# Optimization experiments

Measured on AMD Instinct MI355X. Metric: run time of the kernel, lower is better.

Reference implementation:

```python
import jax, jax.numpy as jnp
import numpy as np

D = 512; H = 8; DFF = 2048; S1 = 1024; S2 = 512; B = 8; EPS = 1e-5


def setup_inputs() -> dict:
    key = jax.random.key(0)
    ks = jax.random.split(key, 10)
    def w(k, shape):
        return jax.random.normal(k, shape, dtype=jnp.float32) * 0.02
    return {
        "rna_embed": jax.random.normal(ks[0], (S1, B, D), dtype=jnp.float32),
        "protein_embed": jax.random.normal(ks[1], (S2, B, D), dtype=jnp.float32),
        # self-attention params (torch MHA packed in_proj)
        "Wqkv_s": w(ks[2], (3 * D, D)), "bqkv_s": jnp.zeros((3 * D,), jnp.float32),
        "Wo_s": w(ks[3], (D, D)), "bo_s": jnp.zeros((D,), jnp.float32),
        # cross-attention params
        "Wqkv_c": w(ks[4], (3 * D, D)), "bqkv_c": jnp.zeros((3 * D,), jnp.float32),
        "Wo_c": w(ks[5], (D, D)), "bo_c": jnp.zeros((D,), jnp.float32),
        # FFN params
        "W1": w(ks[6], (DFF, D)), "b1": jnp.zeros((DFF,), jnp.float32),
        "W2": w(ks[7], (D, DFF)), "b2": jnp.zeros((D,), jnp.float32),
        # LayerNorm params: norm0_1, norm1_1, norm1_2, norm2
        "g0": jnp.ones((D,), jnp.float32), "be0": jnp.zeros((D,), jnp.float32),
        "g11": jnp.ones((D,), jnp.float32), "be11": jnp.zeros((D,), jnp.float32),
        "g12": jnp.ones((D,), jnp.float32), "be12": jnp.zeros((D,), jnp.float32),
        "g2": jnp.ones((D,), jnp.float32), "be2": jnp.zeros((D,), jnp.float32),
    }


def _layernorm(x, g, b):
    m = jnp.mean(x, axis=-1, keepdims=True)
    v = jnp.mean(jnp.square(x - m), axis=-1, keepdims=True)
    return (x - m) * jax.lax.rsqrt(v + EPS) * g + b


def _mha(xq, xkv, Wqkv, bqkv, Wo, bo):
    # xq: (Sq, B, D), xkv: (Sk, B, D)
    Wq, Wk, Wv = jnp.split(Wqkv, 3, axis=0)
    bq, bk, bv = jnp.split(bqkv, 3)
    hd = D // H
    scale = 1.0 / np.sqrt(hd).astype(np.float32)
    q = (xq @ Wq.T + bq).reshape(xq.shape[0], -1, H, hd)   # (Sq,B,H,hd)
    k = (xkv @ Wk.T + bk).reshape(xkv.shape[0], -1, H, hd)  # (Sk,B,H,hd)
    v = (xkv @ Wv.T + bv).reshape(xkv.shape[0], -1, H, hd)
    scores = jnp.einsum('qbhd,kbhd->bhqk', q, k) * scale    # (B,H,Sq,Sk)
    attn = jax.nn.softmax(scores, axis=-1)
    o = jnp.einsum('bhqk,kbhd->qbhd', attn, v).reshape(xq.shape[0], -1, D)
    return o @ Wo.T + bo


def reference(rna_embed, protein_embed, Wqkv_s, bqkv_s, Wo_s, bo_s,
              Wqkv_c, bqkv_c, Wo_c, bo_c, W1, b1, W2, b2,
              g0, be0, g11, be11, g12, be12, g2, be2):
    x1 = rna_embed
    # pre-norm self-attention
    h = _layernorm(x1, g0, be0)
    x1 = x1 + _mha(h, h, Wqkv_s, bqkv_s, Wo_s, bo_s)
    # pre-norm cross-attention (queries from x1, keys/values from protein)
    x1 = x1 + _mha(_layernorm(x1, g11, be11), _layernorm(protein_embed, g12, be12),
                   Wqkv_c, bqkv_c, Wo_c, bo_c)
    # pre-norm FFN
    h = _layernorm(x1, g2, be2)
    x1 = x1 + (jax.nn.relu(h @ W1.T + b1) @ W2.T + b2)
    return x1
```

## Files before the change

kernel.cpp:

```cpp
#include <hip/hip_runtime.h>

typedef unsigned short u16;
typedef unsigned int u32;
typedef u16 u16x8 __attribute__((ext_vector_type(8)));
typedef u16 u16x4 __attribute__((ext_vector_type(4)));
typedef short bfx8 __attribute__((ext_vector_type(8)));
typedef float f32x4 __attribute__((ext_vector_type(4)));

#define AS1 __attribute__((address_space(1)))
#define AS3 __attribute__((address_space(3)))

__device__ __forceinline__ u16 f2bf(float f) {
  union { float f; u32 u; } c; c.f = f;
  u32 u = c.u;
  u += 0x7fffu + ((u >> 16) & 1u);
  return (u16)(u >> 16);
}

__device__ __forceinline__ u32 cvt_pk_bf16(float lo, float hi) {
  u32 r;
  asm("v_cvt_pk_bf16_f32 %0, %1, %2" : "=v"(r) : "v"(lo), "v"(hi));
  return r;
}

__device__ __forceinline__ float fexp2(float x) {
  float r;
  asm("v_exp_f32 %0, %1" : "=v"(r) : "v"(x));
  return r;
}

__device__ __forceinline__ void ln_row(const float* __restrict__ x,
                                       const float* __restrict__ g,
                                       const float* __restrict__ be,
                                       u16* __restrict__ out, int gw, int lane) {
  const float4* row = (const float4*)(x + (size_t)gw * 512);
  float4 a = row[2 * lane], b = row[2 * lane + 1];
  float s = a.x + a.y + a.z + a.w + b.x + b.y + b.z + b.w;
  float q = a.x*a.x + a.y*a.y + a.z*a.z + a.w*a.w + b.x*b.x + b.y*b.y + b.z*b.z + b.w*b.w;
#pragma unroll
  for (int m = 1; m < 64; m <<= 1) { s += __shfl_xor(s, m); q += __shfl_xor(q, m); }
  float mean = s * (1.f / 512.f);
  float var = q * (1.f / 512.f) - mean * mean;
  float rs = rsqrtf(var + 1e-5f);
  const float4* g4 = (const float4*)g;
  const float4* b4 = (const float4*)be;
  float4 ga = g4[2 * lane], gb = g4[2 * lane + 1];
  float4 ba = b4[2 * lane], bb = b4[2 * lane + 1];
  u16x8 o;
  o[0] = f2bf((a.x - mean) * rs * ga.x + ba.x);
  o[1] = f2bf((a.y - mean) * rs * ga.y + ba.y);
  o[2] = f2bf((a.z - mean) * rs * ga.z + ba.z);
  o[3] = f2bf((a.w - mean) * rs * ga.w + ba.w);
  o[4] = f2bf((b.x - mean) * rs * gb.x + bb.x);
  o[5] = f2bf((b.y - mean) * rs * gb.y + bb.y);
  o[6] = f2bf((b.z - mean) * rs * gb.z + bb.z);
  o[7] = f2bf((b.w - mean) * rs * gb.w + bb.w);
  ((u16x8*)(out + (size_t)gw * 512))[lane] = o;
}

__global__ __launch_bounds__(256) void cvtln_kernel(const float* __restrict__ a0, const float* __restrict__ a1,
                                                    const float* __restrict__ a2, const float* __restrict__ a3,
                                                    const float* __restrict__ a4, const float* __restrict__ a5,
                                                    u16* __restrict__ b0, u16* __restrict__ b1,
                                                    u16* __restrict__ b2, u16* __restrict__ b3,
                                                    u16* __restrict__ b4, u16* __restrict__ b5,
                                                    const float* __restrict__ x, const float* __restrict__ g,
                                                    const float* __restrict__ be, u16* __restrict__ lnout) {
  if (blockIdx.x < 4096) {
    int i = blockIdx.x * 256 + threadIdx.x;
    const float* s; u16* d; int off;
    if      (i < 196608) { s = a0; d = b0; off = i; }
    else if (i < 262144) { s = a1; d = b1; off = i - 196608; }
    else if (i < 458752) { s = a2; d = b2; off = i - 262144; }
    else if (i < 524288) { s = a3; d = b3; off = i - 458752; }
    else if (i < 786432) { s = a4; d = b4; off = i - 524288; }
    else                 { s = a5; d = b5; off = i - 786432; }
    float4 v = ((const float4*)s)[off];
    u16x4 o;
    o[0] = f2bf(v.x); o[1] = f2bf(v.y); o[2] = f2bf(v.z); o[3] = f2bf(v.w);
    ((u16x4*)d)[off] = o;
  } else {
    int gw = ((blockIdx.x - 4096) * 256 + threadIdx.x) >> 6;
    ln_row(x, g, be, lnout, gw, threadIdx.x & 63);
  }
}

__global__ __launch_bounds__(256) void ln_kernel(const float* __restrict__ x,
                                                 const float* __restrict__ g,
                                                 const float* __restrict__ be,
                                                 u16* __restrict__ out, int ntok) {
  int gw = (blockIdx.x * 256 + threadIdx.x) >> 6;
  if (gw >= ntok) return;
  ln_row(x, g, be, out, gw, threadIdx.x & 63);
}

__global__ __launch_bounds__(256) void ln2_kernel(const float* __restrict__ xa, const float* __restrict__ ga,
                                                  const float* __restrict__ ba, u16* __restrict__ oa,
                                                  const float* __restrict__ xb, const float* __restrict__ gb,
                                                  const float* __restrict__ bb, u16* __restrict__ ob) {
  int lane = threadIdx.x & 63;
  if (blockIdx.x < 2048) {
    int gw = (blockIdx.x * 256 + threadIdx.x) >> 6;
    ln_row(xa, ga, ba, oa, gw, lane);
  } else {
    int gw = ((blockIdx.x - 2048) * 256 + threadIdx.x) >> 6;
    ln_row(xb, gb, bb, ob, gw, lane);
  }
}

__global__ __launch_bounds__(256) void vt_kernel(const u16* __restrict__ vB, u16* __restrict__ vt,
                                                 int stride, int S) {
  __shared__ u16 lt[64 * 68];
  const int t = threadIdx.x;
  const int b = blockIdx.y, h = blockIdx.z;
  const int sr = t >> 3, dc = (t & 7) * 8;
#pragma unroll
  for (int p = 0; p < 2; ++p) {
    int s = blockIdx.x * 64 + sr + p * 32;
    u16x8 v = *(const u16x8*)(vB + (size_t)(s * 8 + b) * stride + h * 64 + dc);
    u16x4 lo, hi;
    lo[0]=v[0]; lo[1]=v[1]; lo[2]=v[2]; lo[3]=v[3];
    hi[0]=v[4]; hi[1]=v[5]; hi[2]=v[6]; hi[3]=v[7];
    *(u16x4*)&lt[(sr + p * 32) * 68 + dc] = lo;
    *(u16x4*)&lt[(sr + p * 32) * 68 + dc + 4] = hi;
  }
  __syncthreads();
#pragma unroll
  for (int p = 0; p < 2; ++p) {
    int d = sr + p * 32;
    u16x8 o;
#pragma unroll
    for (int e = 0; e < 8; ++e) o[e] = lt[(dc + e) * 68 + d];
    *(u16x8*)(vt + ((size_t)(b * 8 + h) * 64 + d) * S + blockIdx.x * 64 + dc) = o;
  }
}

template <int EPI, int BM, int BN, int MINW>
__global__ __launch_bounds__(512, MINW) void gemm8(const u16* __restrict__ A,
                                                   const u16* __restrict__ Bw,
                                                   const float* __restrict__ bias,
                                                   const float* __restrict__ res,
                                                   void* __restrict__ Cout,
                                                   int N, int M, int K) {
  constexpr int WCg = BN / 64;
  constexpr int WRg = 8 / WCg;
  constexpr int RPW = BM / WRg;
  constexpr int IM = RPW / 16;
  constexpr int LD = (BM + BN) / 64;
  __shared__ __align__(16) u16 lA[2][BM * 64];
  __shared__ __align__(16) u16 lB[2][BN * 64];
  const int tid = threadIdx.x;
  const int lane = tid & 63, w = tid >> 6;
  const int wr = w / WCg, wc = w % WCg;
  const int nwg = gridDim.x * gridDim.y;
  const int id = blockIdx.y * gridDim.x + blockIdx.x;
  const int swz = (id & 7) * (nwg >> 3) + (id >> 3);
  const int bn = (swz / gridDim.x) * BM;
  const int bm = (swz % gridDim.x) * BN;
  const int r15 = lane & 15, kg = lane >> 4;
  const int xr = (r15 & 7) << 4;

  f32x4 acc[IM][4] = {};

  const int lrw = tid >> 3;
  const int lcl = ((tid & 7) * 8) ^ ((lrw & 7) * 8);
  const u16* gA = A + (size_t)(bn + lrw) * K + lcl;
  const u16* gB = Bw + (size_t)(bm + lrw) * K + lcl;
  const int ldsbase = (w * 8) * 64;

#define STAGE8(buf, t) do {                                                               \
    _Pragma("unroll")                                                                     \
    for (int i_ = 0; i_ < BM / 64; ++i_)                                                  \
      __builtin_amdgcn_global_load_lds((AS1 u32*)(gA + (size_t)(i_ * 64) * K + (t) * 64), \
                                       (AS3 u32*)&lA[buf][i_ * 4096 + ldsbase], 16, 0, 0);\
    _Pragma("unroll")                                                                     \
    for (int i_ = 0; i_ < BN / 64; ++i_)                                                  \
      __builtin_amdgcn_global_load_lds((AS1 u32*)(gB + (size_t)(i_ * 64) * K + (t) * 64), \
                                       (AS3 u32*)&lB[buf][i_ * 4096 + ldsbase], 16, 0, 0);\
  } while (0)

  const int nk = K >> 6;
  STAGE8(0, 0);
  for (int t = 0; t < nk; ++t) {
    const int cur = t & 1;
    if (t + 1 < nk) {
      STAGE8(cur ^ 1, t + 1);
      if constexpr (LD == 3)      asm volatile("s_waitcnt vmcnt(3)" ::: "memory");
      else if constexpr (LD == 4) asm volatile("s_waitcnt vmcnt(4)" ::: "memory");
      else                        asm volatile("s_waitcnt vmcnt(8)" ::: "memory");
    } else {
      asm volatile("s_waitcnt vmcnt(0)" ::: "memory");
    }
    __builtin_amdgcn_sched_barrier(0);
    __builtin_amdgcn_s_barrier();
    __builtin_amdgcn_sched_barrier(0);

    const char* Ac = (const char*)lA[cur];
    const char* Bc = (const char*)lB[cur];
    __builtin_amdgcn_s_setprio(1);
#pragma unroll
    for (int kk = 0; kk < 2; ++kk) {
      bfx8 a[IM], b[4];
#pragma unroll
      for (int i = 0; i < IM; ++i)
        a[i] = *(const bfx8*)(Ac + (wr * RPW + i * 16 + r15) * 128 + ((kk * 64 + kg * 16) ^ xr));
#pragma unroll
      for (int j = 0; j < 4; ++j)
        b[j] = *(const bfx8*)(Bc + (wc * 64 + j * 16 + r15) * 128 + ((kk * 64 + kg * 16) ^ xr));
#pragma unroll
      for (int i = 0; i < IM; ++i)
#pragma unroll
        for (int j = 0; j < 4; ++j)
          acc[i][j] = __builtin_amdgcn_mfma_f32_16x16x32_bf16(a[i], b[j], acc[i][j], 0, 0, 0);
    }
    __builtin_amdgcn_s_setprio(0);
    __builtin_amdgcn_sched_barrier(0);
    __builtin_amdgcn_s_barrier();
  }
#undef STAGE8

#pragma unroll
  for (int i = 0; i < IM; ++i) {
#pragma unroll
    for (int j = 0; j < 4; ++j) {
      int col = bm + wc * 64 + j * 16 + r15;
      float bv = bias[col];
#pragma unroll
      for (int r = 0; r < 4; ++r) {
        int row = bn + wr * RPW + i * 16 + kg * 4 + r;
        float v = acc[i][j][r] + bv;
        if (EPI == 1) v = fmaxf(v, 0.f);
        if (EPI == 2) {
          ((float*)Cout)[(size_t)row * M + col] = res[(size_t)row * M + col] + v;
        } else {
          ((u16*)Cout)[(size_t)row * M + col] = f2bf(v);
        }
      }
    }
  }
}

__global__ __launch_bounds__(512, 4) void attn_kernel(const u16* __restrict__ qB,
                                                      const u16* __restrict__ kB,
                                                      const u16* __restrict__ vtB,
                                                      u16* __restrict__ oB,
                                                      int qStride, int kvStride, int Sk) {
  __shared__ __align__(16) u16 lK[4][64 * 64];
  __shared__ __align__(16) u16 lVt[4][64 * 64];
  __shared__ __align__(16) u16 lP[8][16 * 64];
  const int tid = threadIdx.x, lane = tid & 63, w = tid >> 6;
  const int sid = blockIdx.x;
  const int h = sid & 7, b = (sid >> 3) & 7, qt = sid >> 6;
  const int r15 = lane & 15, kg = lane >> 4;
  const int srow = lane >> 3;
  const int sxcol = ((lane & 7) * 8) ^ (srow * 8);

  const int qs = qt * 128 + w * 16 + r15;
  const u16* qrow = qB + (size_t)(qs * 8 + b) * qStride + h * 64;
  bfx8 qf0 = *(const bfx8*)(qrow + kg * 8);
  bfx8 qf1 = *(const bfx8*)(qrow + 32 + kg * 8);

  const u16* vbase = vtB + ((size_t)(b * 8 + h) * 64) * Sk;
  const u16* kp0 = kB + ((size_t)(w * 8 + srow) * 8 + b) * kvStride + h * 64 + sxcol;
  const size_t kAdv = (size_t)64 * 8 * kvStride;
  const u16* vp0 = vbase + (size_t)(w * 8 + srow) * Sk + sxcol;

#define STAGE(buf, tt) do {                                                           \
    __builtin_amdgcn_global_load_lds((AS1 u32*)(kp0 + (size_t)(tt) * kAdv),           \
                                     (AS3 u32*)&lK[buf][(w * 8) * 64], 16, 0, 0);     \
    __builtin_amdgcn_global_load_lds((AS1 u32*)(vp0 + (size_t)(tt) * 64),             \
                                     (AS3 u32*)&lVt[buf][(w * 8) * 64], 16, 0, 0);    \
  } while (0)

  const int nt = Sk / 64;
  const int np = nt >> 1;
  STAGE(0, 0); STAGE(1, 1); STAGE(2, 2); STAGE(3, 3);

  f32x4 oacc[4] = {};
  float mrow = -1e30f, lsum = 0.f;
  const float C2 = 0.125f * 1.44269504088896340736f;
  const int xr = (r15 & 7) << 4;
  char* myP = (char*)lP[w];

  for (int i = 0; i < np; ++i) {
    const int ba = (2 * i) & 3, bb = (2 * i + 1) & 3;
    if (i + 1 < np) { asm volatile("s_waitcnt vmcnt(4)" ::: "memory"); }
    else            { asm volatile("s_waitcnt vmcnt(0)" ::: "memory"); }
    __builtin_amdgcn_sched_barrier(0);
    __builtin_amdgcn_s_barrier();
    __builtin_amdgcn_sched_barrier(0);

    const char* Ka = (const char*)lK[ba];
    const char* Kb = (const char*)lK[bb];
    f32x4 sa[4] = {}, sb[4] = {};
    __builtin_amdgcn_s_setprio(1);
#pragma unroll
    for (int j = 0; j < 4; ++j) {
      const char* kpa = Ka + (j * 16 + r15) * 128;
      bfx8 ka0 = *(const bfx8*)(kpa + ((kg * 16) ^ xr));
      bfx8 ka1 = *(const bfx8*)(kpa + ((64 + kg * 16) ^ xr));
      sa[j] = __builtin_amdgcn_mfma_f32_16x16x32_bf16(ka0, qf0, sa[j], 0, 0, 0);
      sa[j] = __builtin_amdgcn_mfma_f32_16x16x32_bf16(ka1, qf1, sa[j], 0, 0, 0);
    }
#pragma unroll
    for (int j = 0; j < 4; ++j) {
      const char* kpb = Kb + (j * 16 + r15) * 128;
      bfx8 kb0 = *(const bfx8*)(kpb + ((kg * 16) ^ xr));
      bfx8 kb1 = *(const bfx8*)(kpb + ((64 + kg * 16) ^ xr));
      sb[j] = __builtin_amdgcn_mfma_f32_16x16x32_bf16(kb0, qf0, sb[j], 0, 0, 0);
      sb[j] = __builtin_amdgcn_mfma_f32_16x16x32_bf16(kb1, qf1, sb[j], 0, 0, 0);
    }
    __builtin_amdgcn_s_setprio(0);

    float ma = fmaxf(fmaxf(fmaxf(sa[0][0], sa[0][1]), fmaxf(sa[0][2], sa[0][3])),
                     fmaxf(fmaxf(sa[1][0], sa[1][1]), fmaxf(sa[1][2], sa[1][3])));
    float ma2 = fmaxf(fmaxf(fmaxf(sa[2][0], sa[2][1]), fmaxf(sa[2][2], sa[2][3])),
                      fmaxf(fmaxf(sa[3][0], sa[3][1]), fmaxf(sa[3][2], sa[3][3])));
    float mb = fmaxf(fmaxf(fmaxf(sb[0][0], sb[0][1]), fmaxf(sb[0][2], sb[0][3])),
                     fmaxf(fmaxf(sb[1][0], sb[1][1]), fmaxf(sb[1][2], sb[1][3])));
    float mb2 = fmaxf(fmaxf(fmaxf(sb[2][0], sb[2][1]), fmaxf(sb[2][2], sb[2][3])),
                      fmaxf(fmaxf(sb[3][0], sb[3][1]), fmaxf(sb[3][2], sb[3][3])));
    float m0 = fmaxf(fmaxf(ma, ma2), fmaxf(mb, mb2));
    m0 = fmaxf(m0, __shfl_xor(m0, 16));
    m0 = fmaxf(m0, __shfl_xor(m0, 32));

    if (!__all(m0 <= mrow + 16.0f)) {
      float mn = fmaxf(mrow, m0);
      float corr = fexp2((mrow - mn) * C2);
      mrow = mn;
      lsum *= corr;
#pragma unroll
      for (int jd = 0; jd < 4; ++jd)
#pragma unroll
        for (int r = 0; r < 4; ++r) oacc[jd][r] *= corr;
    }
    float bc = -mrow * C2;

    float pa[4][4], pb[4][4];
#pragma unroll
    for (int j = 0; j < 4; ++j)
#pragma unroll
      for (int r = 0; r < 4; ++r) {
        pa[j][r] = fexp2(fmaf(sa[j][r], C2, bc));
        pb[j][r] = fexp2(fmaf(sb[j][r], C2, bc));
      }

    float ps = 0.f;
#pragma unroll
    for (int j = 0; j < 4; ++j)
#pragma unroll
      for (int r = 0; r < 4; ++r) ps += pa[j][r] + pb[j][r];
    ps += __shfl_xor(ps, 16);
    ps += __shfl_xor(ps, 32);
    lsum += ps;

#pragma unroll
    for (int j = 0; j < 4; ++j)
#pragma unroll
      for (int h2 = 0; h2 < 2; ++h2) {
        u32 pk = cvt_pk_bf16(pa[j][2 * h2], pa[j][2 * h2 + 1]);
        int k0b = (j * 16 + kg * 4 + 2 * h2) * 2;
        *(u32*)(myP + r15 * 128 + (k0b ^ xr)) = pk;
      }
    const char* Va = (const char*)lVt[ba];
    __builtin_amdgcn_s_setprio(1);
#pragma unroll
    for (int s2 = 0; s2 < 2; ++s2) {
      bfx8 ptf = *(const bfx8*)(myP + r15 * 128 + ((s2 * 64 + kg * 16) ^ xr));
#pragma unroll
      for (int jd = 0; jd < 4; ++jd) {
        const char* vp = Va + (jd * 16 + r15) * 128;
        bfx8 vf = *(const bfx8*)(vp + ((s2 * 64 + kg * 16) ^ xr));
        oacc[jd] = __builtin_amdgcn_mfma_f32_16x16x32_bf16(vf, ptf, oacc[jd], 0, 0, 0);
      }
    }
    __builtin_amdgcn_s_setprio(0);

#pragma unroll
    for (int j = 0; j < 4; ++j)
#pragma unroll
      for (int h2 = 0; h2 < 2; ++h2) {
        u32 pk = cvt_pk_bf16(pb[j][2 * h2], pb[j][2 * h2 + 1]);
        int k0b = (j * 16 + kg * 4 + 2 * h2) * 2;
        *(u32*)(myP + r15 * 128 + (k0b ^ xr)) = pk;
      }
    const char* Vb = (const char*)lVt[bb];
    __builtin_amdgcn_s_setprio(1);
#pragma unroll
    for (int s2 = 0; s2 < 2; ++s2) {
      bfx8 ptf = *(const bfx8*)(myP + r15 * 128 + ((s2 * 64 + kg * 16) ^ xr));
#pragma unroll
      for (int jd = 0; jd < 4; ++jd) {
        const char* vp = Vb + (jd * 16 + r15) * 128;
        bfx8 vf = *(const bfx8*)(vp + ((s2 * 64 + kg * 16) ^ xr));
        oacc[jd] = __builtin_amdgcn_mfma_f32_16x16x32_bf16(vf, ptf, oacc[jd], 0, 0, 0);
      }
    }
    __builtin_amdgcn_s_setprio(0);

    __builtin_amdgcn_sched_barrier(0);
    __builtin_amdgcn_s_barrier();
    __builtin_amdgcn_sched_barrier(0);
    if (2 * i + 4 < nt) { STAGE(ba, 2 * i + 4); STAGE(bb, 2 * i + 5); }
  }
#undef STAGE

  float inv = 1.f / lsum;
  const int s = qt * 128 + w * 16 + r15;
  u16* orow = oB + (size_t)(s * 8 + b) * 512 + h * 64;
#pragma unroll
  for (int jd = 0; jd < 4; ++jd) {
    u32 p0 = cvt_pk_bf16(oacc[jd][0] * inv, oacc[jd][1] * inv);
    u32 p1 = cvt_pk_bf16(oacc[jd][2] * inv, oacc[jd][3] * inv);
    *(u32*)(orow + jd * 16 + kg * 4) = p0;
    *(u32*)(orow + jd * 16 + kg * 4 + 2) = p1;
  }
}

extern "C" void kernel_launch(void* const* d_in, const int* in_sizes, int n_in,
                              void* d_out, int out_size, void* d_ws, size_t ws_size,
                              hipStream_t stream) {
  const float* rna    = (const float*)d_in[0];
  const float* prot   = (const float*)d_in[1];
  const float* Wqkv_s = (const float*)d_in[2];
  const float* bqkv_s = (const float*)d_in[3];
  const float* Wo_s   = (const float*)d_in[4];
  const float* bo_s   = (const float*)d_in[5];
  const float* Wqkv_c = (const float*)d_in[6];
  const float* bqkv_c = (const float*)d_in[7];
  const float* Wo_c   = (const float*)d_in[8];
  const float* bo_c   = (const float*)d_in[9];
  const float* W1     = (const float*)d_in[10];
  const float* b1     = (const float*)d_in[11];
  const float* W2     = (const float*)d_in[12];
  const float* b2     = (const float*)d_in[13];
  const float* g0  = (const float*)d_in[14];
  const float* be0 = (const float*)d_in[15];
  const float* g11 = (const float*)d_in[16];
  const float* be11= (const float*)d_in[17];
  const float* g12 = (const float*)d_in[18];
  const float* be12= (const float*)d_in[19];
  const float* g2  = (const float*)d_in[20];
  const float* be2 = (const float*)d_in[21];
  float* out = (float*)d_out;

  u16* wbf      = (u16*)d_ws;
  u16* w_qkv_s  = wbf;
  u16* w_o_s    = wbf + 786432;
  u16* w_qkv_c  = wbf + 1048576;
  u16* w_o_c    = wbf + 1835008;
  u16* w_1      = wbf + 2097152;
  u16* w_2      = wbf + 3145728;
  u16* hbuf     = wbf + 4194304;
  u16* qkv      = hbuf + 4194304;
  u16* kvc      = qkv + 4194304;
  u16* attnO    = qkv + 12582912;
  u16* hp       = attnO + 4194304;
  u16* ffnmid   = qkv;

  cvtln_kernel<<<6144, 256, 0, stream>>>(Wqkv_s, Wo_s, Wqkv_c, Wo_c, W1, W2,
                                         w_qkv_s, w_o_s, w_qkv_c, w_o_c, w_1, w_2,
                                         rna, g0, be0, hbuf);

  gemm8<0, 256, 256, 2><<<dim3(6, 32), 512, 0, stream>>>(hbuf, w_qkv_s, bqkv_s, nullptr, qkv, 8192, 1536, 512);
  vt_kernel<<<dim3(16, 8, 8), 256, 0, stream>>>(qkv + 1024, hbuf, 1536, 1024);
  attn_kernel<<<512, 512, 0, stream>>>(qkv, qkv + 512, hbuf, attnO, 1536, 1536, 1024);
  gemm8<2, 64, 128, 6><<<dim3(4, 128), 512, 0, stream>>>(attnO, w_o_s, bo_s, rna, out, 8192, 512, 512);

  ln2_kernel<<<3072, 256, 0, stream>>>(out, g11, be11, hbuf, prot, g12, be12, hp);
  gemm8<0, 64, 128, 6><<<dim3(4, 128), 512, 0, stream>>>(hbuf, w_qkv_c, bqkv_c, nullptr, qkv, 8192, 512, 512);
  gemm8<0, 64, 128, 6><<<dim3(8, 64), 512, 0, stream>>>(hp, w_qkv_c + 512 * 512, bqkv_c + 512, nullptr, kvc, 4096, 1024, 512);
  vt_kernel<<<dim3(8, 8, 8), 256, 0, stream>>>(kvc + 512, hp, 1024, 512);
  attn_kernel<<<512, 512, 0, stream>>>(qkv, kvc, hp, attnO, 512, 1024, 512);
  gemm8<2, 64, 128, 6><<<dim3(4, 128), 512, 0, stream>>>(attnO, w_o_c, bo_c, out, out, 8192, 512, 512);

  ln_kernel<<<2048, 256, 0, stream>>>(out, g2, be2, hbuf, 8192);
  gemm8<1, 256, 256, 2><<<dim3(8, 32), 512, 0, stream>>>(hbuf, w_1, b1, nullptr, ffnmid, 8192, 2048, 512);
  gemm8<2, 64, 128, 6><<<dim3(4, 128), 512, 0, stream>>>(ffnmid, w_2, b2, out, out, 8192, 512, 2048);
}
```

Before: 204.3 us.

## Merge cross-attn Q and KV GEMMs into one launch; restructure attention pipeline

Merges the cross-attention Q projection and KV projection GEMMs into a single dual-problem kernel launch, which removes one launch and its tail. The attention kernel moves from four K/V buffers with prefetch issued at the end of each iteration to two double-buffered pairs prefetched right after the top barrier, dropping one barrier per iteration. It also defers the cross-lane max shuffle into the rare rescale branch and moves the row-sum shuffle reduction out of the loop to the end. The new prefetch order gives less lookahead, and the lazy max reduction relies on the threshold check using only the per-lane max.

```diff
diff --git a/kernel.cpp b/kernel.cpp
--- a/kernel.cpp
+++ b/kernel.cpp
@@ -135,13 +135,13 @@
   }
 }
 
-template <int EPI, int BM, int BN, int MINW>
-__global__ __launch_bounds__(512, MINW) void gemm8(const u16* __restrict__ A,
-                                                   const u16* __restrict__ Bw,
-                                                   const float* __restrict__ bias,
-                                                   const float* __restrict__ res,
-                                                   void* __restrict__ Cout,
-                                                   int N, int M, int K) {
+template <int EPI, int BM, int BN>
+__device__ __forceinline__ void gemm8_body(const u16* __restrict__ A,
+                                           const u16* __restrict__ Bw,
+                                           const float* __restrict__ bias,
+                                           const float* __restrict__ res,
+                                           void* __restrict__ Cout,
+                                           int M, int K, int bn, int bm) {
   constexpr int WCg = BN / 64;
   constexpr int WRg = 8 / WCg;
   constexpr int RPW = BM / WRg;
@@ -152,11 +152,6 @@
   const int tid = threadIdx.x;
   const int lane = tid & 63, w = tid >> 6;
   const int wr = w / WCg, wc = w % WCg;
-  const int nwg = gridDim.x * gridDim.y;
-  const int id = blockIdx.y * gridDim.x + blockIdx.x;
-  const int swz = (id & 7) * (nwg >> 3) + (id >> 3);
-  const int bn = (swz / gridDim.x) * BM;
-  const int bm = (swz % gridDim.x) * BN;
   const int r15 = lane & 15, kg = lane >> 4;
   const int xr = (r15 & 7) << 4;
 
@@ -238,6 +233,35 @@
       }
     }
   }
+}
+
+template <int EPI, int BM, int BN, int MINW>
+__global__ __launch_bounds__(512, MINW) void gemm8(const u16* __restrict__ A,
+                                                   const u16* __restrict__ Bw,
+                                                   const float* __restrict__ bias,
+                                                   const float* __restrict__ res,
+                                                   void* __restrict__ Cout,
+                                                   int N, int M, int K) {
+  const int nwg = gridDim.x * gridDim.y;
+  const int id = blockIdx.y * gridDim.x + blockIdx.x;
+  const int swz = (id & 7) * (nwg >> 3) + (id >> 3);
+  const int bn = (swz / gridDim.x) * BM;
+  const int bm = (swz % gridDim.x) * BN;
+  gemm8_body<EPI, BM, BN>(A, Bw, bias, res, Cout, M, K, bn, bm);
+}
+
+__global__ __launch_bounds__(512, 6) void gemm8_dual(const u16* __restrict__ A0, const u16* __restrict__ W0,
+                                                     const float* __restrict__ c0, u16* __restrict__ O0,
+                                                     const u16* __restrict__ A1, const u16* __restrict__ W1,
+                                                     const float* __restrict__ c1, u16* __restrict__ O1) {
+  const int id = blockIdx.x;
+  const u16 *A, *Bw; const float* bias; u16* C; int M, gx, lid;
+  if (id < 512) { A = A0; Bw = W0; bias = c0; C = O0; M = 512;  gx = 4; lid = id; }
+  else          { A = A1; Bw = W1; bias = c1; C = O1; M = 1024; gx = 8; lid = id - 512; }
+  const int swz = (lid & 7) * 64 + (lid >> 3);
+  const int bn = (swz / gx) * 64;
+  const int bm = (swz % gx) * 128;
+  gemm8_body<0, 64, 128>(A, Bw, bias, nullptr, C, M, 512, bn, bm);
 }
 
 __global__ __launch_bounds__(512, 4) void attn_kernel(const u16* __restrict__ qB,
@@ -274,7 +298,7 @@
 
   const int nt = Sk / 64;
   const int np = nt >> 1;
-  STAGE(0, 0); STAGE(1, 1); STAGE(2, 2); STAGE(3, 3);
+  STAGE(0, 0); STAGE(1, 1);
 
   f32x4 oacc[4] = {};
   float mrow = -1e30f, lsum = 0.f;
@@ -283,16 +307,22 @@
   char* myP = (char*)lP[w];
 
   for (int i = 0; i < np; ++i) {
-    const int ba = (2 * i) & 3, bb = (2 * i + 1) & 3;
-    if (i + 1 < np) { asm volatile("s_waitcnt vmcnt(4)" ::: "memory"); }
-    else            { asm volatile("s_waitcnt vmcnt(0)" ::: "memory"); }
+    const int ba = (i & 1) * 2, bb = ba + 1;
     __builtin_amdgcn_sched_barrier(0);
     __builtin_amdgcn_s_barrier();
     __builtin_amdgcn_sched_barrier(0);
+    if (i + 1 < np) {
+      const int sb = ((i + 1) & 1) * 2;
+      STAGE(sb, 2 * (i + 1)); STAGE(sb + 1, 2 * (i + 1) + 1);
+      asm volatile("s_waitcnt vmcnt(4)" ::: "memory");
+    } else {
+      asm volatile("s_waitcnt vmcnt(0)" ::: "memory");
+    }
+    __builtin_amdgcn_sched_barrier(0);
 
     const char* Ka = (const char*)lK[ba];
     const char* Kb = (const char*)lK[bb];
-    f32x4 sa[4] = {}, sb[4] = {};
+    f32x4 sa[4] = {}, sb_[4] = {};
     __builtin_amdgcn_s_setprio(1);
 #pragma unroll
     for (int j = 0; j < 4; ++j) {
@@ -307,24 +337,24 @@
       const char* kpb = Kb + (j * 16 + r15) * 128;
       bfx8 kb0 = *(const bfx8*)(kpb + ((kg * 16) ^ xr));
       bfx8 kb1 = *(const bfx8*)(kpb + ((64 + kg * 16) ^ xr));
-      sb[j] = __builtin_amdgcn_mfma_f32_16x16x32_bf16(kb0, qf0, sb[j], 0, 0, 0);
-      sb[j] = __builtin_amdgcn_mfma_f32_16x16x32_bf16(kb1, qf1, sb[j], 0, 0, 0);
+      sb_[j] = __builtin_amdgcn_mfma_f32_16x16x32_bf16(kb0, qf0, sb_[j], 0, 0, 0);
+      sb_[j] = __builtin_amdgcn_mfma_f32_16x16x32_bf16(kb1, qf1, sb_[j], 0, 0, 0);
     }
     __builtin_amdgcn_s_setprio(0);
 
-    float ma = fmaxf(fmaxf(fmaxf(sa[0][0], sa[0][1]), fmaxf(sa[0][2], sa[0][3])),
-                     fmaxf(fmaxf(sa[1][0], sa[1][1]), fmaxf(sa[1][2], sa[1][3])));
-    float ma2 = fmaxf(fmaxf(fmaxf(sa[2][0], sa[2][1]), fmaxf(sa[2][2], sa[2][3])),
-                      fmaxf(fmaxf(sa[3][0], sa[3][1]), fmaxf(sa[3][2], sa[3][3])));
-    float mb = fmaxf(fmaxf(fmaxf(sb[0][0], sb[0][1]), fmaxf(sb[0][2], sb[0][3])),
-                     fmaxf(fmaxf(sb[1][0], sb[1][1]), fmaxf(sb[1][2], sb[1][3])));
-    float mb2 = fmaxf(fmaxf(fmaxf(sb[2][0], sb[2][1]), fmaxf(sb[2][2], sb[2][3])),
-                      fmaxf(fmaxf(sb[3][0], sb[3][1]), fmaxf(sb[3][2], sb[3][3])));
-    float m0 = fmaxf(fmaxf(ma, ma2), fmaxf(mb, mb2));
-    m0 = fmaxf(m0, __shfl_xor(m0, 16));
-    m0 = fmaxf(m0, __shfl_xor(m0, 32));
-
-    if (!__all(m0 <= mrow + 16.0f)) {
+    float lm = fmaxf(fmaxf(fmaxf(sa[0][0], sa[0][1]), fmaxf(sa[0][2], sa[0][3])),
+              fmaxf(fmaxf(fmaxf(sa[1][0], sa[1][1]), fmaxf(sa[1][2], sa[1][3])),
+              fmaxf(fmaxf(fmaxf(sa[2][0], sa[2][1]), fmaxf(sa[2][2], sa[2][3])),
+                    fmaxf(fmaxf(sa[3][0], sa[3][1]), fmaxf(sa[3][2], sa[3][3])))));
+    float lmb = fmaxf(fmaxf(fmaxf(sb_[0][0], sb_[0][1]), fmaxf(sb_[0][2], sb_[0][3])),
+               fmaxf(fmaxf(fmaxf(sb_[1][0], sb_[1][1]), fmaxf(sb_[1][2], sb_[1][3])),
+               fmaxf(fmaxf(fmaxf(sb_[2][0], sb_[2][1]), fmaxf(sb_[2][2], sb_[2][3])),
+                     fmaxf(fmaxf(sb_[3][0], sb_[3][1]), fmaxf(sb_[3][2], sb_[3][3])))));
+    lm = fmaxf(lm, lmb);
+
+    if (!__all(lm <= mrow + 16.0f)) {
+      float m0 = fmaxf(lm, __shfl_xor(lm, 16));
+      m0 = fmaxf(m0, __shfl_xor(m0, 32));
       float mn = fmaxf(mrow, m0);
       float corr = fexp2((mrow - mn) * C2);
       mrow = mn;
@@ -342,16 +372,13 @@
 #pragma unroll
       for (int r = 0; r < 4; ++r) {
         pa[j][r] = fexp2(fmaf(sa[j][r], C2, bc));
-        pb[j][r] = fexp2(fmaf(sb[j][r], C2, bc));
+        pb[j][r] = fexp2(fmaf(sb_[j][r], C2, bc));
       }
-
     float ps = 0.f;
 #pragma unroll
     for (int j = 0; j < 4; ++j)
 #pragma unroll
       for (int r = 0; r < 4; ++r) ps += pa[j][r] + pb[j][r];
-    ps += __shfl_xor(ps, 16);
-    ps += __shfl_xor(ps, 32);
     lsum += ps;
 
 #pragma unroll
@@ -397,14 +424,11 @@
       }
     }
     __builtin_amdgcn_s_setprio(0);
-
-    __builtin_amdgcn_sched_barrier(0);
-    __builtin_amdgcn_s_barrier();
-    __builtin_amdgcn_sched_barrier(0);
-    if (2 * i + 4 < nt) { STAGE(ba, 2 * i + 4); STAGE(bb, 2 * i + 5); }
   }
 #undef STAGE
 
+  lsum += __shfl_xor(lsum, 16);
+  lsum += __shfl_xor(lsum, 32);
   float inv = 1.f / lsum;
   const int s = qt * 128 + w * 16 + r15;
   u16* orow = oB + (size_t)(s * 8 + b) * 512 + h * 64;
@@ -468,8 +492,8 @@
   gemm8<2, 64, 128, 6><<<dim3(4, 128), 512, 0, stream>>>(attnO, w_o_s, bo_s, rna, out, 8192, 512, 512);
 
   ln2_kernel<<<3072, 256, 0, stream>>>(out, g11, be11, hbuf, prot, g12, be12, hp);
-  gemm8<0, 64, 128, 6><<<dim3(4, 128), 512, 0, stream>>>(hbuf, w_qkv_c, bqkv_c, nullptr, qkv, 8192, 512, 512);
-  gemm8<0, 64, 128, 6><<<dim3(8, 64), 512, 0, stream>>>(hp, w_qkv_c + 512 * 512, bqkv_c + 512, nullptr, kvc, 4096, 1024, 512);
+  gemm8_dual<<<1024, 512, 0, stream>>>(hbuf, w_qkv_c, bqkv_c, qkv,
+                                       hp, w_qkv_c + 512 * 512, bqkv_c + 512, kvc);
   vt_kernel<<<dim3(8, 8, 8), 256, 0, stream>>>(kvc + 512, hp, 1024, 512);
   attn_kernel<<<512, 512, 0, stream>>>(qkv, kvc, hp, attnO, 512, 1024, 512);
   gemm8<2, 64, 128, 6><<<dim3(4, 128), 512, 0, stream>>>(attnO, w_o_c, bo_c, out, out, 8192, 512, 512);
```

After: 201.5 us. No clear change (-1.3%).
